# Kernel optimization log

Measured on AMD Instinct MI355X. Metric: run time of the kernel, lower is better.

Reference implementation:

```python
import jax, jax.numpy as jnp
import numpy as np

WIN = (7, 7)
NUM_HEADS = 12
DIM = 384
NW = 64        # windows per image
B = 64         # images
B_ = NW * B    # 4096 windows total
N = WIN[0] * WIN[1]  # 49 tokens per window


def _relative_position_index(win):
    wh, ww = win
    coords = np.stack(np.meshgrid(np.arange(wh), np.arange(ww), indexing='ij'))  # (2, wh, ww)
    flat = coords.reshape(2, -1)                                   # (2, N)
    rel = flat[:, :, None] - flat[:, None, :]                      # (2, N, N)
    rel = rel.transpose(1, 2, 0).astype(np.int32)                  # (N, N, 2)
    rel[:, :, 0] += wh - 1
    rel[:, :, 1] += ww - 1
    rel[:, :, 0] *= 2 * ww - 1
    return jnp.asarray(rel.sum(-1), dtype=jnp.int32)               # (N, N)


def setup_inputs() -> dict:
    key = jax.random.key(0)
    ks = jax.random.split(key, 6)
    table_rows = (2 * WIN[0] - 1) * (2 * WIN[1] - 1)  # 169
    return {
        'x': jax.random.normal(ks[0], (B_, N, DIM), dtype=jnp.float32),
        'mask': jnp.zeros((NW, N, N), dtype=jnp.float32),  # 0/-inf additive mask
        'qkv_w': jax.random.normal(ks[1], (3 * DIM, DIM), dtype=jnp.float32) * 0.02,
        'qkv_b': jax.random.normal(ks[2], (3 * DIM,), dtype=jnp.float32) * 0.02,
        'proj_w': jax.random.normal(ks[3], (DIM, DIM), dtype=jnp.float32) * 0.02,
        'proj_b': jax.random.normal(ks[4], (DIM,), dtype=jnp.float32) * 0.02,
        'bias_table': jax.random.normal(ks[5], (table_rows, NUM_HEADS), dtype=jnp.float32) * 0.02,
        'rel_index': _relative_position_index(WIN),
    }


def reference(x, mask, qkv_w, qkv_b, proj_w, proj_b, bias_table, rel_index):
    B_, N, C = x.shape
    H = NUM_HEADS
    hd = C // H
    scale = jnp.asarray(hd, x.dtype) ** -0.5

    qkv = x @ qkv_w.T + qkv_b                              # (B_, N, 3C)
    qkv = qkv.reshape(B_, N, 3, H, hd).transpose(2, 0, 3, 1, 4)  # (3, B_, H, N, hd)
    q, k, v = qkv[0], qkv[1], qkv[2]

    attn = jnp.einsum('bhnd,bhmd->bhnm', q * scale, k)     # (B_, H, N, N)

    # gather relative-position bias: (N*N, H) -> (H, N, N)
    bias = bias_table[rel_index.reshape(-1)].reshape(N, N, H).transpose(2, 0, 1)
    attn = attn + bias[None]

    nW = mask.shape[0]
    attn = attn.reshape(B_ // nW, nW, H, N, N) + mask[None, :, None]
    attn = attn.reshape(B_, H, N, N)

    attn = jax.nn.softmax(attn, axis=-1)

    out = jnp.einsum('bhnm,bhmd->bhnd', attn, v)           # (B_, H, N, hd)
    out = out.transpose(0, 2, 1, 3).reshape(B_, N, C)
    return out @ proj_w.T + proj_b
```

## Files before the change

### kernel.cpp

```cpp
#include <hip/hip_runtime.h>
#include <stdint.h>

#define DIMC   384
#define NHEAD  12
#define HD     32
#define NTOK   49
#define BWIN   4096
#define NROWS  (BWIN * NTOK)
#define K3     (3 * DIMC)

typedef __bf16    bf16x8 __attribute__((ext_vector_type(8)));
typedef _Float16  f16x8  __attribute__((ext_vector_type(8)));
typedef float     f32x4  __attribute__((ext_vector_type(4)));

static __device__ __forceinline__ ushort f2bf(float f) {
    uint32_t u = __float_as_uint(f);
    u += 0x7fffu + ((u >> 16) & 1u);
    return (ushort)(u >> 16);
}
static __device__ __forceinline__ float bf2f(ushort s) {
    return __uint_as_float(((uint32_t)s) << 16);
}
static __device__ __forceinline__ ushort f2h(float f) {
    _Float16 h = (_Float16)f;
    return __builtin_bit_cast(unsigned short, h);
}

static __device__ __forceinline__ void async_ld16(const void* g, void* l) {
    __builtin_amdgcn_global_load_lds(
        (const __attribute__((address_space(1))) void*)g,
        (__attribute__((address_space(3))) void*)l,
        16, 0, 0);
}

__global__ void cvt_f32_bf16(const float* __restrict__ src,
                             ushort* __restrict__ dst, int n4) {
    int i = blockIdx.x * blockDim.x + threadIdx.x;
    int stride = gridDim.x * blockDim.x;
    for (; i < n4; i += stride) {
        float4 v = ((const float4*)src)[i];
        ushort4 o;
        o.x = f2bf(v.x); o.y = f2bf(v.y); o.z = f2bf(v.z); o.w = f2bf(v.w);
        ((ushort4*)dst)[i] = o;
    }
}

template <bool OUT_F32>
__global__ void __launch_bounds__(256)
gemm_bt(const ushort* __restrict__ A, const ushort* __restrict__ Bw,
        const float* __restrict__ bias, void* __restrict__ Cout,
        int M, int Ncols, int K, int scale_cols, float scale_val) {
    __shared__ ushort As[128 * 64];
    __shared__ ushort Bs[128 * 64];

    const int t = threadIdx.x;
    const int nwg   = gridDim.x;
    const int chunk = nwg >> 3;
    const int b0    = blockIdx.x;
    const int swz   = (b0 & 7) * chunk + (b0 >> 3);
    const int nbx   = Ncols >> 7;
    const int bx    = swz % nbx;
    const int by    = swz / nbx;
    const int m0 = by * 128;
    const int n0 = bx * 128;

    const int l  = t & 63;
    const int w  = t >> 6;
    const int wm = w & 1;
    const int wn = w >> 1;

    f32x4 acc[4][4] = {};

    const int rw  = t >> 2;
    const int kc4 = t & 3;
    const ushort* gA = A  + (size_t)(m0 + rw) * K + kc4 * 8;
    const ushort* gB = Bw + (size_t)(n0 + rw) * K + kc4 * 8;
    const size_t rstep = (size_t)64 * K;
    ushort* lA = &As[t * 8];
    ushort* lB = &Bs[t * 8];

    const int fr = l & 15;
    const int kb = (l >> 4) * 8;

    for (int kt = 0; kt < K; kt += 64) {
        async_ld16(gA + kt,             lA);
        async_ld16(gA + kt + rstep,     lA + 2048);
        async_ld16(gA + kt + 32,        lA + 4096);
        async_ld16(gA + kt + 32 + rstep,lA + 6144);
        async_ld16(gB + kt,             lB);
        async_ld16(gB + kt + rstep,     lB + 2048);
        async_ld16(gB + kt + 32,        lB + 4096);
        async_ld16(gB + kt + 32 + rstep,lB + 6144);
        __syncthreads();

#pragma unroll
        for (int s = 0; s < 2; ++s) {
            bf16x8 af[4], bfr[4];
#pragma unroll
            for (int mi = 0; mi < 4; ++mi)
                af[mi] = *(const bf16x8*)&As[s * 4096 + (64 * wm + 16 * mi + fr) * 32 + kb];
#pragma unroll
            for (int ni = 0; ni < 4; ++ni)
                bfr[ni] = *(const bf16x8*)&Bs[s * 4096 + (64 * wn + 16 * ni + fr) * 32 + kb];
#pragma unroll
            for (int mi = 0; mi < 4; ++mi)
#pragma unroll
                for (int ni = 0; ni < 4; ++ni)
                    acc[mi][ni] = __builtin_amdgcn_mfma_f32_16x16x32_bf16(
                        af[mi], bfr[ni], acc[mi][ni], 0, 0, 0);
        }
        __syncthreads();
    }

    const int colBase = n0 + 64 * wn + fr;
    const int rowBase = m0 + 64 * wm + ((l >> 4) << 2);
#pragma unroll
    for (int mi = 0; mi < 4; ++mi) {
#pragma unroll
        for (int ni = 0; ni < 4; ++ni) {
            const int col = colBase + 16 * ni;
            const float bv = bias[col];
            const float sc = (col < scale_cols) ? scale_val : 1.0f;
#pragma unroll
            for (int r = 0; r < 4; ++r) {
                const int row = rowBase + 16 * mi + r;
                const float v = (acc[mi][ni][r] + bv) * sc;
                if (OUT_F32)
                    ((float*)Cout)[(size_t)row * Ncols + col] = v;
                else
                    ((ushort*)Cout)[(size_t)row * Ncols + col] = f2bf(v);
            }
        }
    }
}

__global__ void __launch_bounds__(64)
build_amat(const float* __restrict__ mask, const float* __restrict__ bias_table,
           const int* __restrict__ rel_index, float* __restrict__ amatf) {
    const int h = blockIdx.x;
    const int w = blockIdx.y;
    const int l = threadIdx.x;
    const int q = l >> 4, p = l & 15;
    float4* outp = (float4*)(amatf + (size_t)(w * NHEAD + h) * 4096);
#pragma unroll
    for (int mi = 0; mi < 4; ++mi)
#pragma unroll
        for (int ni = 0; ni < 4; ++ni) {
            float4 v;
            float* vp = (float*)&v;
#pragma unroll
            for (int r = 0; r < 4; ++r) {
                const int i = 16 * mi + 4 * q + r;
                const int j = 16 * ni + p;
                float val;
                if (j >= NTOK)      val = -1e30f;
                else if (i >= NTOK) val = 0.0f;
                else val = bias_table[rel_index[i * NTOK + j] * NHEAD + h]
                         + mask[((size_t)w * NTOK + i) * NTOK + j];
                vp[r] = val;
            }
            outp[(mi * 4 + ni) * 64 + l] = v;
        }
}

__global__ void __launch_bounds__(64)
attn_mfma(const ushort* __restrict__ qkv, const float* __restrict__ amatf,
          ushort* __restrict__ y) {
    const int h = blockIdx.x;
    const int b = blockIdx.y;
    const int w = b & 63;
    __shared__ __align__(16) ushort Ps[64 * 64];
    __shared__ __align__(16) ushort Vs[32 * 64];

    const int l = threadIdx.x;
    const int q = l >> 4;
    const int p = l & 15;
    const size_t rowbase = (size_t)b * NTOK * K3;
    const int kb = q * 8;

    bf16x8 qf[4], kf[4];
#pragma unroll
    for (int mi = 0; mi < 4; ++mi) {
        const int iu = 16 * mi + p;
        const int i  = iu > 48 ? 48 : iu;
        qf[mi] = *(const bf16x8*)(qkv + rowbase + (size_t)i * K3 + h * HD + kb);
    }
#pragma unroll
    for (int ni = 0; ni < 4; ++ni) {
        const int ju = 16 * ni + p;
        const int j  = ju > 48 ? 48 : ju;
        kf[ni] = *(const bf16x8*)(qkv + rowbase + (size_t)j * K3 + DIMC + h * HD + kb);
    }
    uint4 vch[4];
#pragma unroll
    for (int it = 0; it < 4; ++it) {
        const int c  = l + it * 64;
        const int ju = c >> 2, dc = c & 3;
        const int j  = ju > 48 ? 48 : ju;
        vch[it] = *(const uint4*)(qkv + rowbase + (size_t)j * K3 + 2 * DIMC + h * HD + dc * 8);
    }

    f32x4 acc[4][4] = {};
#pragma unroll
    for (int mi = 0; mi < 4; ++mi)
#pragma unroll
        for (int ni = 0; ni < 4; ++ni)
            acc[mi][ni] = __builtin_amdgcn_mfma_f32_16x16x32_bf16(
                qf[mi], kf[ni], acc[mi][ni], 0, 0, 0);

    const float4* ap = (const float4*)(amatf + (size_t)(w * NHEAD + h) * 4096);
#pragma unroll
    for (int mi = 0; mi < 4; ++mi)
#pragma unroll
        for (int ni = 0; ni < 4; ++ni) {
            const float4 am = ap[(mi * 4 + ni) * 64 + l];
            acc[mi][ni][0] += am.x; acc[mi][ni][1] += am.y;
            acc[mi][ni][2] += am.z; acc[mi][ni][3] += am.w;
        }

    float inv[4][4];
#pragma unroll
    for (int mi = 0; mi < 4; ++mi) {
        float mrow[4];
#pragma unroll
        for (int r = 0; r < 4; ++r) {
            float m = fmaxf(fmaxf(acc[mi][0][r], acc[mi][1][r]),
                            fmaxf(acc[mi][2][r], acc[mi][3][r]));
            m = fmaxf(m, __shfl_xor(m, 1));
            m = fmaxf(m, __shfl_xor(m, 2));
            m = fmaxf(m, __shfl_xor(m, 4));
            m = fmaxf(m, __shfl_xor(m, 8));
            mrow[r] = m;
        }
        float rsum[4] = {0.f, 0.f, 0.f, 0.f};
#pragma unroll
        for (int ni = 0; ni < 4; ++ni)
#pragma unroll
            for (int r = 0; r < 4; ++r) {
                const float e = __expf(acc[mi][ni][r] - mrow[r]);
                acc[mi][ni][r] = e;
                rsum[r] += e;
            }
#pragma unroll
        for (int r = 0; r < 4; ++r) {
            float s = rsum[r];
            s += __shfl_xor(s, 1);
            s += __shfl_xor(s, 2);
            s += __shfl_xor(s, 4);
            s += __shfl_xor(s, 8);
            inv[mi][r] = __builtin_amdgcn_rcpf(s);
        }
    }

#pragma unroll
    for (int mi = 0; mi < 4; ++mi)
#pragma unroll
        for (int ni = 0; ni < 4; ++ni)
#pragma unroll
            for (int r = 0; r < 4; ++r) {
                const int row = 16 * mi + 4 * q + r;
                const int off = (row * 128 + (16 * ni + p) * 2) ^ ((row & 7) << 4);
                *(ushort*)((char*)Ps + off) = f2h(acc[mi][ni][r]);
            }
#pragma unroll
    for (int it = 0; it < 4; ++it) {
        const int c  = l + it * 64;
        const int ju = c >> 2, dc = c & 3;
        const ushort* vsrc = (const ushort*)&vch[it];
#pragma unroll
        for (int e = 0; e < 8; ++e) {
            const int d   = dc * 8 + e;
            const int off = (d * 128 + ju * 2) ^ (((d >> 3) & 1) << 6);
            *(ushort*)((char*)Vs + off) = f2h(bf2f(vsrc[e]));
        }
    }
    __syncthreads();

    f32x4 o[4][2] = {};
#pragma unroll
    for (int kk = 0; kk < 2; ++kk) {
        f16x8 pa[4], vb[2];
#pragma unroll
        for (int mi = 0; mi < 4; ++mi) {
            const int row = 16 * mi + p;
            const int off = (row * 128 + kk * 64 + q * 16) ^ ((row & 7) << 4);
            pa[mi] = *(const f16x8*)((const char*)Ps + off);
        }
#pragma unroll
        for (int ni = 0; ni < 2; ++ni) {
            const int d   = 16 * ni + p;
            const int off = (d * 128 + kk * 64 + q * 16) ^ (((d >> 3) & 1) << 6);
            vb[ni] = *(const f16x8*)((const char*)Vs + off);
        }
#pragma unroll
        for (int mi = 0; mi < 4; ++mi)
#pragma unroll
            for (int ni = 0; ni < 2; ++ni)
                o[mi][ni] = __builtin_amdgcn_mfma_f32_16x16x32_f16(
                    pa[mi], vb[ni], o[mi][ni], 0, 0, 0);
    }

    ushort* yb = y + (size_t)b * NTOK * DIMC + h * HD;
#pragma unroll
    for (int mi = 0; mi < 4; ++mi)
#pragma unroll
        for (int r = 0; r < 4; ++r) {
            const int i = 16 * mi + 4 * q + r;
            if (i < NTOK) {
                const float s = inv[mi][r];
                yb[(size_t)i * DIMC + p]      = f2bf(o[mi][0][r] * s);
                yb[(size_t)i * DIMC + 16 + p] = f2bf(o[mi][1][r] * s);
            }
        }
}

extern "C" void kernel_launch(void* const* d_in, const int* in_sizes, int n_in,
                              void* d_out, int out_size, void* d_ws, size_t ws_size,
                              hipStream_t stream) {
    const float* x          = (const float*)d_in[0];
    const float* mask       = (const float*)d_in[1];
    const float* qkv_w      = (const float*)d_in[2];
    const float* qkv_b      = (const float*)d_in[3];
    const float* proj_w     = (const float*)d_in[4];
    const float* proj_b     = (const float*)d_in[5];
    const float* bias_table = (const float*)d_in[6];
    const int*   rel_index  = (const int*)d_in[7];

    ushort* ws   = (ushort*)d_ws;
    ushort* xb   = ws;
    ushort* wqkv = ws + (size_t)77070336;
    ushort* wprj = ws + (size_t)77070336 + 442368;
    ushort* qkvb = ws + (size_t)77070336 + 442368 + 147456;
    float*  amat = (float*)(ws + (size_t)308871168);

    cvt_f32_bf16<<<4096, 256, 0, stream>>>(x, xb, (NROWS * DIMC) / 4);
    cvt_f32_bf16<<<432, 256, 0, stream>>>(qkv_w, wqkv, (K3 * DIMC) / 4);
    cvt_f32_bf16<<<144, 256, 0, stream>>>(proj_w, wprj, (DIMC * DIMC) / 4);
    build_amat<<<dim3(NHEAD, 64), 64, 0, stream>>>(mask, bias_table, rel_index, amat);

    gemm_bt<false><<<(K3 / 128) * (NROWS / 128), 256, 0, stream>>>(
        xb, wqkv, qkv_b, qkvb, NROWS, K3, DIMC, DIMC, 0.17677669529663687f);

    attn_mfma<<<dim3(NHEAD, BWIN), 64, 0, stream>>>(qkvb, amat, xb);

    gemm_bt<true><<<(DIMC / 128) * (NROWS / 128), 256, 0, stream>>>(
        xb, wprj, proj_b, d_out, NROWS, DIMC, DIMC, 0, 1.0f);
}
```

Baseline: 1.187 ms.

## Keep full-K weight tile resident in LDS and stream A fragments from global

Replaces the K-looped 128x128 GEMM with a 256x64 tile kernel. The kernel loads the whole 64xK weight slice into XOR-swizzled LDS once, then each wave reads its A fragments straight from global memory into registers with double buffering. This removes the per-K-step LDS staging of A and the per-step barriers, and raises occupancy with launch bounds of 3 blocks. In exchange there is no LDS reuse of A across waves and each fragment load is a small global access, which relies on cache hits. K is hardcoded to 384.

```diff
diff --git a/kernel.cpp b/kernel.cpp
--- a/kernel.cpp
+++ b/kernel.cpp
@@ -8,6 +8,7 @@
 #define BWIN   4096
 #define NROWS  (BWIN * NTOK)
 #define K3     (3 * DIMC)
+#define GK     384
 
 typedef __bf16    bf16x8 __attribute__((ext_vector_type(8)));
 typedef _Float16  f16x8  __attribute__((ext_vector_type(8)));
@@ -24,13 +25,6 @@
 static __device__ __forceinline__ ushort f2h(float f) {
     _Float16 h = (_Float16)f;
     return __builtin_bit_cast(unsigned short, h);
-}
-
-static __device__ __forceinline__ void async_ld16(const void* g, void* l) {
-    __builtin_amdgcn_global_load_lds(
-        (const __attribute__((address_space(1))) void*)g,
-        (__attribute__((address_space(3))) void*)l,
-        16, 0, 0);
 }
 
 __global__ void cvt_f32_bf16(const float* __restrict__ src,
@@ -46,81 +40,85 @@
 }
 
 template <bool OUT_F32>
-__global__ void __launch_bounds__(256)
-gemm_bt(const ushort* __restrict__ A, const ushort* __restrict__ Bw,
-        const float* __restrict__ bias, void* __restrict__ Cout,
-        int M, int Ncols, int K, int scale_cols, float scale_val) {
-    __shared__ ushort As[128 * 64];
-    __shared__ ushort Bs[128 * 64];
+__global__ void __launch_bounds__(256, 3)
+gemm_bres(const ushort* __restrict__ A, const ushort* __restrict__ Bw,
+          const float* __restrict__ bias, void* __restrict__ Cout,
+          int M, int Ncols, int scale_cols, float scale_val) {
+    __shared__ ushort Bs[64 * GK];
 
     const int t = threadIdx.x;
     const int nwg   = gridDim.x;
     const int chunk = nwg >> 3;
     const int b0    = blockIdx.x;
     const int swz   = (b0 & 7) * chunk + (b0 >> 3);
-    const int nbx   = Ncols >> 7;
+    const int nbx   = Ncols >> 6;
     const int bx    = swz % nbx;
     const int by    = swz / nbx;
-    const int m0 = by * 128;
-    const int n0 = bx * 128;
+    const int m0 = by * 256;
+    const int n0 = bx * 64;
 
     const int l  = t & 63;
     const int w  = t >> 6;
-    const int wm = w & 1;
-    const int wn = w >> 1;
+    const int fr = l & 15;
+    const int q4 = l >> 4;
+    const int kb = q4 * 8;
+
+    {
+        const int row = t >> 2;
+        const int c0  = (t & 3) * 12;
+        const ushort* g = Bw + (size_t)(n0 + row) * GK;
+#pragma unroll
+        for (int c = 0; c < 12; ++c) {
+            const int slot = c0 + c;
+            uint4 v = *(const uint4*)(g + slot * 8);
+            const int byte = (row * 768 + slot * 16) ^ ((row & 7) << 4);
+            *(uint4*)((char*)Bs + byte) = v;
+        }
+    }
+    __syncthreads();
+
+    const ushort* gA = A + (size_t)(m0 + 64 * w + fr) * GK + kb;
 
     f32x4 acc[4][4] = {};
-
-    const int rw  = t >> 2;
-    const int kc4 = t & 3;
-    const ushort* gA = A  + (size_t)(m0 + rw) * K + kc4 * 8;
-    const ushort* gB = Bw + (size_t)(n0 + rw) * K + kc4 * 8;
-    const size_t rstep = (size_t)64 * K;
-    ushort* lA = &As[t * 8];
-    ushort* lB = &Bs[t * 8];
-
-    const int fr = l & 15;
-    const int kb = (l >> 4) * 8;
-
-    for (int kt = 0; kt < K; kt += 64) {
-        async_ld16(gA + kt,             lA);
-        async_ld16(gA + kt + rstep,     lA + 2048);
-        async_ld16(gA + kt + 32,        lA + 4096);
-        async_ld16(gA + kt + 32 + rstep,lA + 6144);
-        async_ld16(gB + kt,             lB);
-        async_ld16(gB + kt + rstep,     lB + 2048);
-        async_ld16(gB + kt + 32,        lB + 4096);
-        async_ld16(gB + kt + 32 + rstep,lB + 6144);
-        __syncthreads();
-
-#pragma unroll
-        for (int s = 0; s < 2; ++s) {
-            bf16x8 af[4], bfr[4];
+    bf16x8 af[2][4];
+
+#pragma unroll
+    for (int mi = 0; mi < 4; ++mi)
+        af[0][mi] = *(const bf16x8*)(gA + (size_t)16 * mi * GK);
+
+#pragma unroll
+    for (int ks = 0; ks < 12; ++ks) {
+        const int cur = ks & 1;
+        const int nxt = cur ^ 1;
+        if (ks < 11) {
 #pragma unroll
             for (int mi = 0; mi < 4; ++mi)
-                af[mi] = *(const bf16x8*)&As[s * 4096 + (64 * wm + 16 * mi + fr) * 32 + kb];
+                af[nxt][mi] = *(const bf16x8*)(gA + (size_t)16 * mi * GK + (ks + 1) * 32);
+        }
+        bf16x8 bfr[4];
+#pragma unroll
+        for (int ni = 0; ni < 4; ++ni) {
+            const int n = 16 * ni + fr;
+            bfr[ni] = *(const bf16x8*)((const char*)Bs +
+                        ((n * 768 + ks * 64 + q4 * 16) ^ ((n & 7) << 4)));
+        }
+#pragma unroll
+        for (int mi = 0; mi < 4; ++mi)
 #pragma unroll
             for (int ni = 0; ni < 4; ++ni)
-                bfr[ni] = *(const bf16x8*)&Bs[s * 4096 + (64 * wn + 16 * ni + fr) * 32 + kb];
-#pragma unroll
-            for (int mi = 0; mi < 4; ++mi)
-#pragma unroll
-                for (int ni = 0; ni < 4; ++ni)
-                    acc[mi][ni] = __builtin_amdgcn_mfma_f32_16x16x32_bf16(
-                        af[mi], bfr[ni], acc[mi][ni], 0, 0, 0);
-        }
-        __syncthreads();
-    }
-
-    const int colBase = n0 + 64 * wn + fr;
-    const int rowBase = m0 + 64 * wm + ((l >> 4) << 2);
-#pragma unroll
-    for (int mi = 0; mi < 4; ++mi) {
-#pragma unroll
-        for (int ni = 0; ni < 4; ++ni) {
-            const int col = colBase + 16 * ni;
-            const float bv = bias[col];
-            const float sc = (col < scale_cols) ? scale_val : 1.0f;
+                acc[mi][ni] = __builtin_amdgcn_mfma_f32_16x16x32_bf16(
+                    af[cur][mi], bfr[ni], acc[mi][ni], 0, 0, 0);
+    }
+
+    const int colBase = n0 + fr;
+    const int rowBase = m0 + 64 * w + (q4 << 2);
+#pragma unroll
+    for (int ni = 0; ni < 4; ++ni) {
+        const int col = colBase + 16 * ni;
+        const float bv = bias[col];
+        const float sc = (col < scale_cols) ? scale_val : 1.0f;
+#pragma unroll
+        for (int mi = 0; mi < 4; ++mi) {
 #pragma unroll
             for (int r = 0; r < 4; ++r) {
                 const int row = rowBase + 16 * mi + r;
@@ -338,11 +336,11 @@
     cvt_f32_bf16<<<144, 256, 0, stream>>>(proj_w, wprj, (DIMC * DIMC) / 4);
     build_amat<<<dim3(NHEAD, 64), 64, 0, stream>>>(mask, bias_table, rel_index, amat);
 
-    gemm_bt<false><<<(K3 / 128) * (NROWS / 128), 256, 0, stream>>>(
-        xb, wqkv, qkv_b, qkvb, NROWS, K3, DIMC, DIMC, 0.17677669529663687f);
+    gemm_bres<false><<<(K3 / 64) * (NROWS / 256), 256, 0, stream>>>(
+        xb, wqkv, qkv_b, qkvb, NROWS, K3, DIMC, 0.17677669529663687f);
 
     attn_mfma<<<dim3(NHEAD, BWIN), 64, 0, stream>>>(qkvb, amat, xb);
 
-    gemm_bt<true><<<(DIMC / 128) * (NROWS / 128), 256, 0, stream>>>(
-        xb, wprj, proj_b, d_out, NROWS, DIMC, DIMC, 0, 1.0f);
-}
+    gemm_bres<true><<<(DIMC / 64) * (NROWS / 256), 256, 0, stream>>>(
+        xb, wprj, proj_b, d_out, NROWS, DIMC, 0, 1.0f);
+}
```

Measured after the change: 1.420 ms. 1.2x slower.
